# Performance work log

Hardware: AMD Instinct MI355X
Metric: run time of the kernel (lower is better)

The kernel has to match this reference:

```python
import jax, jax.numpy as jnp
import numpy as np

NUM_PITCHES = 128
RHYTHM_DIM = 10
HARMONY_DIM = 12
VOCAB_SIZE = 390
EPS = 1e-08


def setup_inputs() -> dict:
    key = jax.random.key(0)
    k_tok, k_w1, k_w2 = jax.random.split(key, 3)
    B, T = 1024, 8192
    stats_dim = NUM_PITCHES + RHYTHM_DIM + HARMONY_DIM  # 150
    midi_tokens = jax.random.randint(k_tok, (B, T), 0, VOCAB_SIZE, dtype=jnp.int64 if jax.config.jax_enable_x64 else jnp.int32)
    W1 = jax.random.normal(k_w1, (stats_dim, 256), dtype=jnp.float32) * 0.05
    b1 = jnp.zeros((256,), dtype=jnp.float32)
    W2 = jax.random.normal(k_w2, (256, 128), dtype=jnp.float32) * 0.05
    b2 = jnp.zeros((128,), dtype=jnp.float32)
    return {"midi_tokens": midi_tokens, "W1": W1, "b1": b1, "W2": W2, "b2": b2}


def _compute_stats(midi_tokens):
    """Vectorized pitch histogram + rhythm + harmony stats. midi_tokens: (B, T) int."""
    B, T = midi_tokens.shape
    # Pitch distribution: histogram of tokens % 128 per batch row, via one flat scatter-add.
    pitch = midi_tokens % NUM_PITCHES  # (B, T) in [0, 128)
    flat_bins = (jnp.arange(B, dtype=pitch.dtype)[:, None] * NUM_PITCHES + pitch).reshape(-1)
    hist = jnp.zeros((B * NUM_PITCHES,), dtype=jnp.float32).at[flat_bins].add(1.0)
    pitch_dist = hist.reshape(B, NUM_PITCHES)
    pitch_dist = pitch_dist / (pitch_dist.sum(axis=-1, keepdims=True) + EPS)
    # Rhythm: mean and (unbiased, torch-default) std; remaining 8 dims are zeros.
    tf = midi_tokens.astype(jnp.float32)
    mean = tf.mean(axis=-1)
    std = jnp.sqrt(((tf - mean[:, None]) ** 2).sum(axis=-1) / (T - 1))
    rhythm = jnp.zeros((B, RHYTHM_DIM), dtype=jnp.float32)
    rhythm = rhythm.at[:, 0].set(mean).at[:, 1].set(std)
    # Harmony: original uses torch.rand(12) per row; deterministic uniform here.
    harmony = jax.random.uniform(jax.random.key(42), (B, HARMONY_DIM), dtype=jnp.float32)
    return jnp.concatenate([pitch_dist, rhythm, harmony], axis=-1)  # (B, 150)


def reference(midi_tokens, W1, b1, W2, b2):
    stats = _compute_stats(midi_tokens)
    h = jax.nn.relu(stats @ W1 + b1)
    return h @ W2 + b2  # (B, feature_dim=128)
```

## Files before the change

kernel.cpp:

```cpp
#include <hip/hip_runtime.h>
#include <stdint.h>
#include <math.h>

#define SEQ_T 8192
#define STATS_STRIDE 160

__device__ __forceinline__ uint32_t rotl32(uint32_t x, int n) {
    return (x << n) | (x >> (32 - n));
}

__device__ uint32_t jax_threefry_bits_12288(uint32_t idx) {
    const uint32_t k0 = 0u, k1 = 42u, k2 = 0u ^ 42u ^ 0x1BD11BDAu;
    uint32_t i = (idx < 6144u) ? idx : (idx - 6144u);
    uint32_t x0 = i + k0;
    uint32_t x1 = (i + 6144u) + k1;
#define TF_R4(a,b,c,d) \
    x0 += x1; x1 = rotl32(x1, a); x1 ^= x0; \
    x0 += x1; x1 = rotl32(x1, b); x1 ^= x0; \
    x0 += x1; x1 = rotl32(x1, c); x1 ^= x0; \
    x0 += x1; x1 = rotl32(x1, d); x1 ^= x0;
    TF_R4(13, 15, 26, 6);   x0 += k1; x1 += k2 + 1u;
    TF_R4(17, 29, 16, 24);  x0 += k2; x1 += k0 + 2u;
    TF_R4(13, 15, 26, 6);   x0 += k0; x1 += k1 + 3u;
    TF_R4(17, 29, 16, 24);  x0 += k1; x1 += k2 + 4u;
    TF_R4(13, 15, 26, 6);   x0 += k2; x1 += k0 + 5u;
#undef TF_R4
    return (idx < 6144u) ? x0 : x1;
}

__global__ __launch_bounds__(256) void stats_kernel(const int* __restrict__ tok,
                                                    float* __restrict__ stats) {
    const int b = blockIdx.x;
    const int tid = threadIdx.x;
    const int wave = tid >> 6;

    __shared__ int hist[4][128];
    __shared__ int wsum[4];
    __shared__ unsigned wsq[4];

    for (int i = tid; i < 512; i += 256) ((int*)hist)[i] = 0;
    __syncthreads();

    const int4* tp = (const int4*)(tok + (size_t)b * SEQ_T);
    int sum = 0;
    unsigned sq = 0;
#pragma unroll
    for (int j = 0; j < 8; ++j) {
        int4 v = tp[j * 256 + tid];
        atomicAdd(&hist[wave][v.x & 127], 1); sum += v.x; sq += (unsigned)(v.x * v.x);
        atomicAdd(&hist[wave][v.y & 127], 1); sum += v.y; sq += (unsigned)(v.y * v.y);
        atomicAdd(&hist[wave][v.z & 127], 1); sum += v.z; sq += (unsigned)(v.z * v.z);
        atomicAdd(&hist[wave][v.w & 127], 1); sum += v.w; sq += (unsigned)(v.w * v.w);
    }

#pragma unroll
    for (int off = 32; off > 0; off >>= 1) {
        sum += __shfl_down(sum, off);
        sq  += __shfl_down(sq, off);
    }
    if ((tid & 63) == 0) { wsum[wave] = sum; wsq[wave] = sq; }
    __syncthreads();

    if (tid < 150) {
        float val;
        if (tid < 128) {
            int h = hist[0][tid] + hist[1][tid] + hist[2][tid] + hist[3][tid];
            val = (float)h * (1.0f / 8192.0f);
        } else if (tid == 128) {
            int s = wsum[0] + wsum[1] + wsum[2] + wsum[3];
            val = (float)s * (1.0f / 8192.0f);
        } else if (tid == 129) {
            double s = (double)(wsum[0] + wsum[1] + wsum[2] + wsum[3]);
            double q = (double)wsq[0] + (double)wsq[1] + (double)wsq[2] + (double)wsq[3];
            double var = (q - s * s / 8192.0) / 8191.0;
            val = (float)sqrt(var);
        } else if (tid < 138) {
            val = 0.0f;
        } else {
            uint32_t bits = jax_threefry_bits_12288((uint32_t)b * 12u + (uint32_t)(tid - 138));
            val = __uint_as_float((bits >> 9) | 0x3f800000u) - 1.0f;
        }
        stats[b * STATS_STRIDE + tid] = val;
    }
}

__global__ __launch_bounds__(256) void mlp_kernel(const float* __restrict__ stats,
                                                  const float* __restrict__ W1,
                                                  const float* __restrict__ b1,
                                                  const float* __restrict__ W2,
                                                  const float* __restrict__ b2,
                                                  float* __restrict__ out) {
    __shared__ float s[4][150];
    __shared__ float h[4][256];
    const int tid = threadIdx.x;
    const int rb = blockIdx.x * 4;

    for (int i = tid; i < 600; i += 256) {
        int r = i / 150, k = i - r * 150;
        s[r][k] = stats[(rb + r) * STATS_STRIDE + k];
    }
    __syncthreads();

    float a0 = b1[tid], a1 = a0, a2 = a0, a3 = a0;
#pragma unroll 5
    for (int k = 0; k < 150; ++k) {
        float w = W1[k * 256 + tid];
        a0 = fmaf(s[0][k], w, a0);
        a1 = fmaf(s[1][k], w, a1);
        a2 = fmaf(s[2][k], w, a2);
        a3 = fmaf(s[3][k], w, a3);
    }
    h[0][tid] = fmaxf(a0, 0.0f);
    h[1][tid] = fmaxf(a1, 0.0f);
    h[2][tid] = fmaxf(a2, 0.0f);
    h[3][tid] = fmaxf(a3, 0.0f);
    __syncthreads();

    const int c = tid & 127, g = tid >> 7;
    const float* h0 = h[g * 2];
    const float* h1 = h[g * 2 + 1];
    float o0 = b2[c], o1 = o0;
#pragma unroll 8
    for (int k = 0; k < 256; ++k) {
        float w = W2[k * 128 + c];
        o0 = fmaf(h0[k], w, o0);
        o1 = fmaf(h1[k], w, o1);
    }
    out[(rb + g * 2) * 128 + c] = o0;
    out[(rb + g * 2 + 1) * 128 + c] = o1;
}

extern "C" void kernel_launch(void* const* d_in, const int* in_sizes, int n_in,
                              void* d_out, int out_size, void* d_ws, size_t ws_size,
                              hipStream_t stream) {
    const int*   tok = (const int*)d_in[0];
    const float* W1  = (const float*)d_in[1];
    const float* b1  = (const float*)d_in[2];
    const float* W2  = (const float*)d_in[3];
    const float* b2  = (const float*)d_in[4];
    float* out   = (float*)d_out;
    float* stats = (float*)d_ws;

    stats_kernel<<<1024, 256, 0, stream>>>(tok, stats);
    mlp_kernel<<<256, 256, 0, stream>>>(stats, W1, b1, W2, b2, out);
}
```

Before: 100.8 us.

## Fuse stats and MLP into one kernel processing two rows per block

Merges the histogram/stats kernel and the MLP kernel into a single launch where each 512-thread block handles two token rows, keeping stats and hidden activations in shared memory instead of a global workspace. Token loads become nontemporal, squares use 24-bit multiplies, and the second layer splits K across two thread halves with a shared-memory reduction. This removes a kernel launch and the workspace round trip. In exchange, each W1/W2 load is reused across only two rows instead of four, which raises weight traffic, and the grid shrinks to 512 blocks.

```diff
diff --git a/kernel.cpp b/kernel.cpp
--- a/kernel.cpp
+++ b/kernel.cpp
@@ -2,8 +2,9 @@
 #include <stdint.h>
 #include <math.h>
 
-#define SEQ_T 8192
-#define STATS_STRIDE 160
+#define T_SEQ 8192
+
+typedef int vint4 __attribute__((ext_vector_type(4)));
 
 __device__ __forceinline__ uint32_t rotl32(uint32_t x, int n) {
     return (x << n) | (x >> (32 - n));
@@ -28,106 +29,96 @@
     return (idx < 6144u) ? x0 : x1;
 }
 
-__global__ __launch_bounds__(256) void stats_kernel(const int* __restrict__ tok,
-                                                    float* __restrict__ stats) {
-    const int b = blockIdx.x;
+__global__ __launch_bounds__(512) void fused_kernel(const int* __restrict__ tok,
+                                                    const float* __restrict__ W1,
+                                                    const float* __restrict__ b1,
+                                                    const float* __restrict__ W2,
+                                                    const float* __restrict__ b2,
+                                                    float* __restrict__ out) {
     const int tid = threadIdx.x;
     const int wave = tid >> 6;
+    const int r0 = blockIdx.x * 2;
 
-    __shared__ int hist[4][128];
-    __shared__ int wsum[4];
-    __shared__ unsigned wsq[4];
+    __shared__ int hist[8][128];
+    __shared__ int wsum[8];
+    __shared__ unsigned wsq[8];
+    __shared__ float s[2][150];
+    __shared__ float h[2][256];
+    __shared__ float part[2][128];
 
-    for (int i = tid; i < 512; i += 256) ((int*)hist)[i] = 0;
+    for (int i = tid; i < 1024; i += 512) ((int*)hist)[i] = 0;
     __syncthreads();
 
-    const int4* tp = (const int4*)(tok + (size_t)b * SEQ_T);
-    int sum = 0;
-    unsigned sq = 0;
+    {
+        const int row_local = tid >> 8;
+        const int t256 = tid & 255;
+        const vint4* tp = (const vint4*)(tok + (size_t)(r0 + row_local) * T_SEQ);
+        int sum = 0;
+        unsigned sq = 0;
 #pragma unroll
-    for (int j = 0; j < 8; ++j) {
-        int4 v = tp[j * 256 + tid];
-        atomicAdd(&hist[wave][v.x & 127], 1); sum += v.x; sq += (unsigned)(v.x * v.x);
-        atomicAdd(&hist[wave][v.y & 127], 1); sum += v.y; sq += (unsigned)(v.y * v.y);
-        atomicAdd(&hist[wave][v.z & 127], 1); sum += v.z; sq += (unsigned)(v.z * v.z);
-        atomicAdd(&hist[wave][v.w & 127], 1); sum += v.w; sq += (unsigned)(v.w * v.w);
-    }
-
+        for (int j = 0; j < 8; ++j) {
+            vint4 v = __builtin_nontemporal_load(&tp[j * 256 + t256]);
+            atomicAdd(&hist[wave][v.x & 127], 1); sum += v.x; sq += (unsigned)__mul24(v.x, v.x);
+            atomicAdd(&hist[wave][v.y & 127], 1); sum += v.y; sq += (unsigned)__mul24(v.y, v.y);
+            atomicAdd(&hist[wave][v.z & 127], 1); sum += v.z; sq += (unsigned)__mul24(v.z, v.z);
+            atomicAdd(&hist[wave][v.w & 127], 1); sum += v.w; sq += (unsigned)__mul24(v.w, v.w);
+        }
 #pragma unroll
-    for (int off = 32; off > 0; off >>= 1) {
-        sum += __shfl_down(sum, off);
-        sq  += __shfl_down(sq, off);
-    }
-    if ((tid & 63) == 0) { wsum[wave] = sum; wsq[wave] = sq; }
-    __syncthreads();
-
-    if (tid < 150) {
-        float val;
-        if (tid < 128) {
-            int h = hist[0][tid] + hist[1][tid] + hist[2][tid] + hist[3][tid];
-            val = (float)h * (1.0f / 8192.0f);
-        } else if (tid == 128) {
-            int s = wsum[0] + wsum[1] + wsum[2] + wsum[3];
-            val = (float)s * (1.0f / 8192.0f);
-        } else if (tid == 129) {
-            double s = (double)(wsum[0] + wsum[1] + wsum[2] + wsum[3]);
-            double q = (double)wsq[0] + (double)wsq[1] + (double)wsq[2] + (double)wsq[3];
-            double var = (q - s * s / 8192.0) / 8191.0;
-            val = (float)sqrt(var);
-        } else if (tid < 138) {
-            val = 0.0f;
-        } else {
-            uint32_t bits = jax_threefry_bits_12288((uint32_t)b * 12u + (uint32_t)(tid - 138));
-            val = __uint_as_float((bits >> 9) | 0x3f800000u) - 1.0f;
+        for (int off = 32; off > 0; off >>= 1) {
+            sum += __shfl_down(sum, off);
+            sq  += __shfl_down(sq, off);
         }
-        stats[b * STATS_STRIDE + tid] = val;
-    }
-}
-
-__global__ __launch_bounds__(256) void mlp_kernel(const float* __restrict__ stats,
-                                                  const float* __restrict__ W1,
-                                                  const float* __restrict__ b1,
-                                                  const float* __restrict__ W2,
-                                                  const float* __restrict__ b2,
-                                                  float* __restrict__ out) {
-    __shared__ float s[4][150];
-    __shared__ float h[4][256];
-    const int tid = threadIdx.x;
-    const int rb = blockIdx.x * 4;
-
-    for (int i = tid; i < 600; i += 256) {
-        int r = i / 150, k = i - r * 150;
-        s[r][k] = stats[(rb + r) * STATS_STRIDE + k];
+        if ((tid & 63) == 0) { wsum[wave] = sum; wsq[wave] = sq; }
     }
     __syncthreads();
 
-    float a0 = b1[tid], a1 = a0, a2 = a0, a3 = a0;
-#pragma unroll 5
-    for (int k = 0; k < 150; ++k) {
-        float w = W1[k * 256 + tid];
-        a0 = fmaf(s[0][k], w, a0);
-        a1 = fmaf(s[1][k], w, a1);
-        a2 = fmaf(s[2][k], w, a2);
-        a3 = fmaf(s[3][k], w, a3);
+    if (tid < 300) {
+        const int r = tid >= 150;
+        const int k = tid - r * 150;
+        const int wb = r * 4;
+        float val;
+        if (k < 128) {
+            int hh = hist[wb][k] + hist[wb + 1][k] + hist[wb + 2][k] + hist[wb + 3][k];
+            val = (float)hh * (1.0f / 8192.0f);
+        } else if (k == 128) {
+            int ss = wsum[wb] + wsum[wb + 1] + wsum[wb + 2] + wsum[wb + 3];
+            val = (float)ss * (1.0f / 8192.0f);
+        } else if (k == 129) {
+            double ss = (double)(wsum[wb] + wsum[wb + 1] + wsum[wb + 2] + wsum[wb + 3]);
+            double qq = (double)wsq[wb] + (double)wsq[wb + 1] + (double)wsq[wb + 2] + (double)wsq[wb + 3];
+            val = (float)sqrt((qq - ss * ss / 8192.0) / 8191.0);
+        } else if (k < 138) {
+            val = 0.0f;
+        } else {
+            uint32_t bits = jax_threefry_bits_12288((uint32_t)(r0 + r) * 12u + (uint32_t)(k - 138));
+            val = __uint_as_float((bits >> 9) | 0x3f800000u) - 1.0f;
+        }
+        s[r][k] = val;
     }
-    h[0][tid] = fmaxf(a0, 0.0f);
-    h[1][tid] = fmaxf(a1, 0.0f);
-    h[2][tid] = fmaxf(a2, 0.0f);
-    h[3][tid] = fmaxf(a3, 0.0f);
     __syncthreads();
 
-    const int c = tid & 127, g = tid >> 7;
-    const float* h0 = h[g * 2];
-    const float* h1 = h[g * 2 + 1];
-    float o0 = b2[c], o1 = o0;
+    {
+        const int g = tid >> 8, c = tid & 255;
+        float acc = b1[c];
+#pragma unroll 5
+        for (int k = 0; k < 150; ++k)
+            acc = fmaf(s[g][k], W1[k * 256 + c], acc);
+        h[g][c] = fmaxf(acc, 0.0f);
+    }
+    __syncthreads();
+
+    {
+        const int half = tid >> 8, g = (tid >> 7) & 1, c = tid & 127;
+        const float* hr = h[g];
+        const int kb = half * 128;
+        float acc = half ? 0.0f : b2[c];
 #pragma unroll 8
-    for (int k = 0; k < 256; ++k) {
-        float w = W2[k * 128 + c];
-        o0 = fmaf(h0[k], w, o0);
-        o1 = fmaf(h1[k], w, o1);
+        for (int k = 0; k < 128; ++k)
+            acc = fmaf(hr[kb + k], W2[(kb + k) * 128 + c], acc);
+        if (half) part[g][c] = acc;
+        __syncthreads();
+        if (!half) out[(r0 + g) * 128 + c] = acc + part[g][c];
     }
-    out[(rb + g * 2) * 128 + c] = o0;
-    out[(rb + g * 2 + 1) * 128 + c] = o1;
 }
 
 extern "C" void kernel_launch(void* const* d_in, const int* in_sizes, int n_in,
@@ -138,9 +129,7 @@
     const float* b1  = (const float*)d_in[2];
     const float* W2  = (const float*)d_in[3];
     const float* b2  = (const float*)d_in[4];
-    float* out   = (float*)d_out;
-    float* stats = (float*)d_ws;
+    float* out = (float*)d_out;
 
-    stats_kernel<<<1024, 256, 0, stream>>>(tok, stats);
-    mlp_kernel<<<256, 256, 0, stream>>>(stats, W1, b1, W2, b2, out);
+    fused_kernel<<<512, 512, 0, stream>>>(tok, W1, b1, W2, b2, out);
 }
```

New measurement: 98.36 us, median of 2. 2.4% less time.
